# Optimization experiments

Hardware: AMD Instinct MI355X
Metric: run time of the kernel (lower is better)

## Reference

```python
import jax, jax.numpy as jnp
import numpy as np

B, LTEXT, LVIS, D, H = 16, 128, 4096, 1024, 16
HD = D // H


def setup_inputs() -> dict:
    key = jax.random.key(0)
    ks = jax.random.split(key, 8)
    s = 0.02
    return {
        'hidden_states': jax.random.normal(ks[0], (B, LVIS, D), jnp.float32),
        'text_states': jax.random.normal(ks[1], (LTEXT, B, D), jnp.float32),
        'Wq': jax.random.normal(ks[2], (D, D), jnp.float32) * s,
        'bq': jnp.zeros((D,), jnp.float32),
        'Wk': jax.random.normal(ks[3], (D, D), jnp.float32) * s,
        'bk': jnp.zeros((D,), jnp.float32),
        'Wv': jax.random.normal(ks[4], (D, D), jnp.float32) * s,
        'bv': jnp.zeros((D,), jnp.float32),
        'Wo': jax.random.normal(ks[5], (D, D), jnp.float32) * s,
        'bo': jnp.zeros((D,), jnp.float32),
    }


def reference(hidden_states, text_states, Wq, bq, Wk, bk, Wv, bv, Wo, bo):
    # text_states: (L_text, B, D) -- code unpacks text_len, bsz from dims 0,1
    # hidden_states: (B, L_vis, D) -- key/value source
    Ltext, bsz, d = text_states.shape
    Lvis = hidden_states.shape[1]
    scale = HD ** -0.5

    # projections (torch Linear x @ W.T + b, here W stored already transposed)
    q = (text_states @ Wq + bq) * scale
    # faithful to torch .view: flatten memory then reshape to (B, Ltext, H, hd)
    q = q.reshape(bsz, Ltext, H, HD).transpose(0, 2, 1, 3)        # (B,H,Lt,hd)
    k = (hidden_states @ Wk + bk).reshape(bsz, Lvis, H, HD).transpose(0, 2, 1, 3)
    v = (hidden_states @ Wv + bv).reshape(bsz, Lvis, H, HD).transpose(0, 2, 1, 3)

    attn = jax.nn.softmax(jnp.einsum('bhtd,bhsd->bhts', q, k), axis=-1)  # (B,H,Lt,Lv)
    text_guided_vision = jnp.einsum('bhts,bhsd->bhtd', attn, v)          # (B,H,Lt,hd)
    # second matmul with transposed attention weights: P^T @ (P V)
    out = jnp.einsum('bhts,bhtd->bhsd', attn, text_guided_vision)        # (B,H,Lv,hd)

    out = out.transpose(0, 2, 1, 3).reshape(bsz, Lvis, d)
    return out @ Wo + bo
```

## Files before the change

### kernel.cpp

```cpp
#include <hip/hip_runtime.h>
#include <stdint.h>

typedef short  s16x8 __attribute__((ext_vector_type(8)));
typedef float  f32x4 __attribute__((ext_vector_type(4)));
typedef unsigned short u16x4 __attribute__((ext_vector_type(4)));

__device__ __forceinline__ unsigned short f2bf(float f) {
  unsigned u = __builtin_bit_cast(unsigned, f);
  u = (u + 0x7fffu + ((u >> 16) & 1u)) >> 16;
  return (unsigned short)u;
}

__device__ __forceinline__ void glds16(const void* g, void* l) {
  __builtin_amdgcn_global_load_lds((const __attribute__((address_space(1))) void*)g,
                                   (__attribute__((address_space(3))) void*)l, 16, 0, 0);
}

__device__ __forceinline__ f32x4 mfma16(s16x8 a, s16x8 b, f32x4 c) {
  return __builtin_amdgcn_mfma_f32_16x16x32_bf16(a, b, c, 0, 0, 0);
}

#define VM4 asm volatile("s_waitcnt vmcnt(4)" ::: "memory")
#define VM0 asm volatile("s_waitcnt vmcnt(0)" ::: "memory")

__global__ __launch_bounds__(256) void kt_cvt(const float* __restrict__ X,
                                              unsigned short* __restrict__ Y) {
  const size_t N8 = (size_t)16 * 4096 * 1024 / 8;
  for (size_t i = (size_t)blockIdx.x * 256 + threadIdx.x; i < N8;
       i += (size_t)gridDim.x * 256) {
    const float* g = X + i * 8;
    f32x4 a = *(const f32x4*)g;
    f32x4 b = *(const f32x4*)(g + 4);
    s16x8 o;
    o[0]=f2bf(a[0]); o[1]=f2bf(a[1]); o[2]=f2bf(a[2]); o[3]=f2bf(a[3]);
    o[4]=f2bf(b[0]); o[5]=f2bf(b[1]); o[6]=f2bf(b[2]); o[7]=f2bf(b[3]);
    *(s16x8*)(Y + i * 8) = o;
  }
}

__global__ void kt_transpose(const float* __restrict__ W, unsigned short* __restrict__ WT) {
  __shared__ float tile[64][65];
  int n0 = blockIdx.x * 64, k0 = blockIdx.y * 64;
  int tx = threadIdx.x, ty = threadIdx.y;
  #pragma unroll
  for (int r = ty; r < 64; r += 4)
    tile[r][tx] = W[(size_t)(k0 + r) * 1024 + n0 + tx];
  __syncthreads();
  #pragma unroll
  for (int r = ty; r < 64; r += 4)
    WT[(size_t)(n0 + r) * 1024 + k0 + tx] = f2bf(tile[tx][r]);
}

__global__ __launch_bounds__(256, 2) void kt_gemm_q(
    const float* __restrict__ Ain, const unsigned short* __restrict__ BT,
    const float* __restrict__ bias, unsigned short* __restrict__ Cout) {
  __shared__ __align__(16) unsigned short As[128 * 32];
  __shared__ __align__(16) unsigned short Bs[128 * 32];
  const int tid = threadIdx.x, lane = tid & 63, wave = tid >> 6;
  const int l15 = lane & 15, quad = lane >> 4;
  const int wr = wave >> 1, wc = wave & 1;
  const int n0 = blockIdx.x * 128, m0 = blockIdx.y * 128;

  f32x4 acc[4][4] = {};
  for (int k0 = 0; k0 < 1024; k0 += 32) {
    __syncthreads();
    #pragma unroll
    for (int i = 0; i < 2; ++i) {
      int rowb = (wave * 2 + i) * 16 + (lane >> 2);
      glds16(BT + (size_t)(n0 + rowb) * 1024 + k0 + (lane & 3) * 8,
             &Bs[(wave * 2 + i) * 512]);
    }
    {
      const float* A = Ain;
      int row = tid >> 1, ks = (tid & 1) * 16;
      const float* g = &A[(size_t)(m0 + row) * 1024 + k0 + ks];
      f32x4 fa = *(const f32x4*)(g);
      f32x4 fb = *(const f32x4*)(g + 4);
      f32x4 fc = *(const f32x4*)(g + 8);
      f32x4 fd = *(const f32x4*)(g + 12);
      s16x8 lo, hi;
      lo[0]=f2bf(fa[0]); lo[1]=f2bf(fa[1]); lo[2]=f2bf(fa[2]); lo[3]=f2bf(fa[3]);
      lo[4]=f2bf(fb[0]); lo[5]=f2bf(fb[1]); lo[6]=f2bf(fb[2]); lo[7]=f2bf(fb[3]);
      hi[0]=f2bf(fc[0]); hi[1]=f2bf(fc[1]); hi[2]=f2bf(fc[2]); hi[3]=f2bf(fc[3]);
      hi[4]=f2bf(fd[0]); hi[5]=f2bf(fd[1]); hi[6]=f2bf(fd[2]); hi[7]=f2bf(fd[3]);
      *(s16x8*)&As[row * 32 + ks] = lo;
      *(s16x8*)&As[row * 32 + ks + 8] = hi;
    }
    __syncthreads();
    s16x8 a[4], b[4];
    #pragma unroll
    for (int i = 0; i < 4; ++i) a[i] = *(const s16x8*)&As[(wr * 64 + i * 16 + l15) * 32 + quad * 8];
    #pragma unroll
    for (int j = 0; j < 4; ++j) b[j] = *(const s16x8*)&Bs[(wc * 64 + j * 16 + l15) * 32 + quad * 8];
    #pragma unroll
    for (int i = 0; i < 4; ++i)
      #pragma unroll
      for (int j = 0; j < 4; ++j) acc[i][j] = mfma16(a[i], b[j], acc[i][j]);
  }
  #pragma unroll
  for (int j = 0; j < 4; ++j) {
    int col = n0 + wc * 64 + j * 16 + l15;
    float bv = bias[col];
    #pragma unroll
    for (int i = 0; i < 4; ++i)
      #pragma unroll
      for (int r = 0; r < 4; ++r) {
        int row = m0 + wr * 64 + i * 16 + quad * 4 + r;
        float v = (acc[i][j][r] + bv) * 0.125f;
        size_t idx = ((size_t)((row >> 7) * 16 + (col >> 6)) * 128 + (row & 127)) * 64 + (col & 63);
        Cout[idx] = f2bf(v);
      }
  }
}

template <int MODE>
__global__ __launch_bounds__(512, 2) void kt_gemm256(
    const unsigned short* __restrict__ A, const unsigned short* __restrict__ BT,
    const float* __restrict__ bias, void* __restrict__ Cout) {
  __shared__ __align__(16) unsigned short lds[65536];
  const int tid = threadIdx.x, lane = tid & 63, wave = tid >> 6;
  const int l15 = lane & 15, quad = lane >> 4;
  const int wr = wave >> 2, wc = wave & 3;
  const int r0 = lane >> 3, sck = (lane & 7) ^ r0;
  const int nblk = blockIdx.x & 3, mblk = blockIdx.x >> 2;
  const int n0 = nblk * 256, m0 = mblk * 256;
  const unsigned short* Asrc = A + (size_t)m0 * 1024;
  const unsigned short* Bsrc = BT + (size_t)n0 * 1024;

  f32x4 acc[8][4] = {};
  s16x8 bf_[4][2];

  auto stageA = [&](int t, int h, int buf) {
    #pragma unroll
    for (int is = 0; is < 2; ++is) {
      int c = wave * 2 + is;
      glds16(Asrc + (size_t)(h * 128 + c * 8 + r0) * 1024 + t * 64 + sck * 8,
             &lds[buf * 32768 + h * 8192 + c * 512]);
    }
  };
  auto stageB = [&](int t, int h, int buf) {
    #pragma unroll
    for (int is = 0; is < 2; ++is) {
      int c = wave * 2 + is;
      glds16(Bsrc + (size_t)(h * 128 + c * 8 + r0) * 1024 + t * 64 + sck * 8,
             &lds[buf * 32768 + 16384 + h * 8192 + c * 512]);
    }
  };

  stageA(0, 0, 0); stageA(0, 1, 0); stageB(0, 0, 0); stageB(0, 1, 0);
  stageB(1, 0, 1); stageB(1, 1, 1);
  VM4;
  __builtin_amdgcn_s_barrier();

  #pragma unroll 1
  for (int it = 0; it < 8; ++it) {
    const bool last = (it == 7);
    const int te = 2 * it;
    #pragma unroll
    for (int half = 0; half < 2; ++half) {
      const int buf = half;
      #pragma unroll
      for (int p = 0; p < 4; ++p) {
        if (p == 0) {
          #pragma unroll
          for (int j = 0; j < 4; ++j)
            #pragma unroll
            for (int kk = 0; kk < 2; ++kk) {
              int r = (wc & 1) * 64 + j * 16 + l15;
              bf_[j][kk] = *(const s16x8*)&lds[buf * 32768 + 16384 + (wc >> 1) * 8192
                                               + r * 64 + (((kk * 4 + quad) ^ (r & 7)) << 3)];
            }
        }
        s16x8 af[2][2];
        #pragma unroll
        for (int ii = 0; ii < 2; ++ii)
          #pragma unroll
          for (int kk = 0; kk < 2; ++kk) {
            int r = (p * 2 + ii) * 16 + l15;
            af[ii][kk] = *(const s16x8*)&lds[buf * 32768 + wr * 8192
                                             + r * 64 + (((kk * 4 + quad) ^ (r & 7)) << 3)];
          }
        if (half == 0) {
          if (p == 0) { stageA(te + 1, 0, 1); stageA(te + 1, 1, 1); }
          else if (p == 1) { if (!last) stageB(te + 2, 0, 0); }
          else if (p == 2) { if (!last) stageB(te + 2, 1, 0); }
        } else {
          if (p == 0) { if (!last) stageA(te + 2, 0, 0); }
          else if (p == 1) { if (!last) { stageA(te + 2, 1, 0); stageB(te + 3, 0, 1); } }
          else if (p == 2) { if (!last) stageB(te + 3, 1, 1); }
        }
        __builtin_amdgcn_s_barrier();
        __builtin_amdgcn_s_setprio(1);
        #pragma unroll
        for (int ii = 0; ii < 2; ++ii)
          #pragma unroll
          for (int j = 0; j < 4; ++j)
            #pragma unroll
            for (int kk = 0; kk < 2; ++kk)
              acc[p * 2 + ii][j] = mfma16(af[ii][kk], bf_[j][kk], acc[p * 2 + ii][j]);
        __builtin_amdgcn_s_setprio(0);
        if (p == 3) {
          if (half == 0) { if (last) { VM0; } else { VM4; } }
          else           { if (!last) { VM4; } }
        }
        __builtin_amdgcn_s_barrier();
      }
    }
  }

  const int bb = m0 >> 12;
  #pragma unroll
  for (int j = 0; j < 4; ++j) {
    const int col = n0 + wc * 64 + j * 16 + l15;
    const float bv = bias[col];
    const int hcol = col >> 6, dcol = col & 63;
    #pragma unroll
    for (int i = 0; i < 8; ++i) {
      const int row0 = m0 + wr * 128 + i * 16 + quad * 4;
      const int s = row0 & 4095;
      if constexpr (MODE == 0) {
        unsigned short* Ko = (unsigned short*)Cout;
        size_t base = (((size_t)bb * 16 + hcol) * 4096 + s) * 64 + dcol;
        #pragma unroll
        for (int r = 0; r < 4; ++r) Ko[base + (size_t)r * 64] = f2bf(acc[i][j][r] + bv);
      } else if constexpr (MODE == 1) {
        size_t base = (((size_t)bb * 16 + hcol) * 64 + dcol) * 4096 + s;
        u16x4 w;
        #pragma unroll
        for (int r = 0; r < 4; ++r) w[r] = f2bf(acc[i][j][r] + bv);
        *(u16x4*)&((unsigned short*)Cout)[base] = w;
      } else {
        float* O = (float*)Cout;
        size_t base = (size_t)row0 * 1024 + col;
        #pragma unroll
        for (int r = 0; r < 4; ++r) O[base + (size_t)r * 1024] = acc[i][j][r] + bv;
      }
    }
  }
}

__global__ __launch_bounds__(256, 2) void kt_attn1(
    const unsigned short* __restrict__ Qb, const unsigned short* __restrict__ Kb,
    const unsigned short* __restrict__ Vt, float* __restrict__ RpT,
    float* __restrict__ Zp) {
  __shared__ __align__(16) unsigned short Ks[128 * 64];
  __shared__ __align__(16) unsigned short Vts[64 * 128];
  __shared__ __align__(16) unsigned short Es[128 * 128];
  const int tid = threadIdx.x, lane = tid & 63, wave = tid >> 6;
  const int l15 = lane & 15, quad = lane >> 4;
  const int qidx = blockIdx.x, h = blockIdx.y, b = blockIdx.z;
  const int bh = b * 16 + h;
  const size_t kbase = (size_t)bh * 4096 * 64;
  const size_t vbase = (size_t)bh * 64 * 4096;
  s16x8 qa[2][2];
  #pragma unroll
  for (int i = 0; i < 2; ++i)
    #pragma unroll
    for (int kk = 0; kk < 2; ++kk)
      qa[i][kk] = *(const s16x8*)&Qb[((size_t)bh * 128 + wave * 32 + i * 16 + l15) * 64 + kk * 32 + quad * 8];
  s16x8 bones;
  { unsigned short o = (l15 == 0) ? (unsigned short)0x3F80 : (unsigned short)0;
    #pragma unroll
    for (int c2 = 0; c2 < 8; ++c2) bones[c2] = (short)o; }
  f32x4 Racc[2][4] = {};
  f32x4 Zacc[2] = {};
  for (int ch = 0; ch < 8; ++ch) {
    const int s0 = qidx * 1024 + ch * 128;
    __syncthreads();
    #pragma unroll
    for (int i = 0; i < 4; ++i) {
      int srow = (wave * 4 + i) * 8 + (lane >> 3);
      glds16(Kb + kbase + (size_t)(s0 + srow) * 64 + (lane & 7) * 8, &Ks[(wave * 4 + i) * 512]);
    }
    #pragma unroll
    for (int i = 0; i < 4; ++i) {
      int drow = (wave * 4 + i) * 4 + (lane >> 4);
      glds16(Vt + vbase + (size_t)drow * 4096 + s0 + (lane & 15) * 8, &Vts[(wave * 4 + i) * 512]);
    }
    __syncthreads();
    f32x4 Sacc[2][8] = {};
    #pragma unroll
    for (int kk = 0; kk < 2; ++kk) {
      s16x8 bk_[8];
      #pragma unroll
      for (int j = 0; j < 8; ++j)
        bk_[j] = *(const s16x8*)&Ks[(j * 16 + l15) * 64 + kk * 32 + quad * 8];
      #pragma unroll
      for (int i = 0; i < 2; ++i)
        #pragma unroll
        for (int j = 0; j < 8; ++j) Sacc[i][j] = mfma16(qa[i][kk], bk_[j], Sacc[i][j]);
    }
    #pragma unroll
    for (int i = 0; i < 2; ++i)
      #pragma unroll
      for (int j = 0; j < 8; ++j)
        #pragma unroll
        for (int r = 0; r < 4; ++r)
          Es[(wave * 32 + i * 16 + quad * 4 + r) * 128 + j * 16 + l15] = f2bf(__expf(Sacc[i][j][r]));
    #pragma unroll
    for (int kk = 0; kk < 4; ++kk) {
      s16x8 ea[2];
      #pragma unroll
      for (int i2 = 0; i2 < 2; ++i2)
        ea[i2] = *(const s16x8*)&Es[(wave * 32 + i2 * 16 + l15) * 128 + kk * 32 + quad * 8];
      s16x8 bv_[4];
      #pragma unroll
      for (int jd = 0; jd < 4; ++jd)
        bv_[jd] = *(const s16x8*)&Vts[(jd * 16 + l15) * 128 + kk * 32 + quad * 8];
      #pragma unroll
      for (int i2 = 0; i2 < 2; ++i2) {
        #pragma unroll
        for (int jd = 0; jd < 4; ++jd) Racc[i2][jd] = mfma16(ea[i2], bv_[jd], Racc[i2][jd]);
        Zacc[i2] = mfma16(ea[i2], bones, Zacc[i2]);
      }
    }
  }
  #pragma unroll
  for (int i2 = 0; i2 < 2; ++i2) {
    int t0 = wave * 32 + i2 * 16 + quad * 4;
    #pragma unroll
    for (int jd = 0; jd < 4; ++jd) {
      int d = jd * 16 + l15;
      *(f32x4*)&RpT[(((size_t)qidx * 256 + bh) * 64 + d) * 128 + t0] = Racc[i2][jd];
    }
    if (l15 == 0) {
      #pragma unroll
      for (int r = 0; r < 4; ++r)
        Zp[((size_t)qidx * 256 + bh) * 128 + t0 + r] = Zacc[i2][r];
    }
  }
}

__global__ void kt_reduce(const float* __restrict__ RpT, const float* __restrict__ Zp,
                          unsigned short* __restrict__ Gt) {
  size_t id = (size_t)blockIdx.x * 256 + threadIdx.x;
  int t = (int)(id & 127);
  size_t bh = id >> 13;
  float z = 0.f, r = 0.f;
  #pragma unroll
  for (int q = 0; q < 4; ++q) {
    z += Zp[(size_t)q * 32768 + bh * 128 + t];
    r += RpT[(size_t)q * 2097152 + id];
  }
  Gt[id] = f2bf(r / (z * z));
}

__global__ __launch_bounds__(256, 2) void kt_attn2(
    const unsigned short* __restrict__ Qb, const unsigned short* __restrict__ Kb,
    const unsigned short* __restrict__ Gt, unsigned short* __restrict__ Ao) {
  __shared__ __align__(16) unsigned short Ks[64 * 64];
  __shared__ __align__(16) unsigned short EsT[64 * 136];
  const int tid = threadIdx.x, lane = tid & 63, wave = tid >> 6;
  const int l15 = lane & 15, quad = lane >> 4;
  const int c = blockIdx.x, h = blockIdx.y, b = blockIdx.z;
  const int bh = b * 16 + h;
  s16x8 qf[8][2], gf[4][4];
  #pragma unroll
  for (int jt = 0; jt < 8; ++jt)
    #pragma unroll
    for (int kk = 0; kk < 2; ++kk)
      qf[jt][kk] = *(const s16x8*)&Qb[((size_t)bh * 128 + jt * 16 + l15) * 64 + kk * 32 + quad * 8];
  #pragma unroll
  for (int jd = 0; jd < 4; ++jd)
    #pragma unroll
    for (int kk = 0; kk < 4; ++kk)
      gf[jd][kk] = *(const s16x8*)&Gt[((size_t)bh * 64 + jd * 16 + l15) * 128 + kk * 32 + quad * 8];
  const size_t kbase = (size_t)bh * 4096 * 64;
  for (int it = 0; it < 16; ++it) {
    const int s0 = c * 1024 + it * 64;
    __syncthreads();
    #pragma unroll
    for (int i = 0; i < 2; ++i) {
      int srow = (wave * 2 + i) * 8 + (lane >> 3);
      glds16(Kb + kbase + (size_t)(s0 + srow) * 64 + (lane & 7) * 8, &Ks[(wave * 2 + i) * 512]);
    }
    __syncthreads();
    f32x4 Sacc[8] = {};
    #pragma unroll
    for (int kk = 0; kk < 2; ++kk) {
      s16x8 a = *(const s16x8*)&Ks[(wave * 16 + l15) * 64 + kk * 32 + quad * 8];
      #pragma unroll
      for (int jt = 0; jt < 8; ++jt) Sacc[jt] = mfma16(a, qf[jt][kk], Sacc[jt]);
    }
    #pragma unroll
    for (int jt = 0; jt < 8; ++jt)
      #pragma unroll
      for (int r = 0; r < 4; ++r)
        EsT[(wave * 16 + quad * 4 + r) * 136 + jt * 16 + l15] = f2bf(__expf(Sacc[jt][r]));
    f32x4 Oacc[4] = {};
    #pragma unroll
    for (int kk = 0; kk < 4; ++kk) {
      s16x8 ea = *(const s16x8*)&EsT[(wave * 16 + l15) * 136 + kk * 32 + quad * 8];
      #pragma unroll
      for (int jd = 0; jd < 4; ++jd) Oacc[jd] = mfma16(ea, gf[jd][kk], Oacc[jd]);
    }
    #pragma unroll
    for (int jd = 0; jd < 4; ++jd)
      #pragma unroll
      for (int r = 0; r < 4; ++r) {
        int s = s0 + wave * 16 + quad * 4 + r;
        int d = jd * 16 + l15;
        Ao[((size_t)b * 4096 + s) * 1024 + h * 64 + d] = f2bf(Oacc[jd][r]);
      }
  }
}

extern "C" void kernel_launch(void* const* d_in, const int* in_sizes, int n_in,
                              void* d_out, int out_size, void* d_ws, size_t ws_size,
                              hipStream_t stream) {
  const float* hidden = (const float*)d_in[0];
  const float* text   = (const float*)d_in[1];
  const float* Wq = (const float*)d_in[2]; const float* bq = (const float*)d_in[3];
  const float* Wk = (const float*)d_in[4]; const float* bk = (const float*)d_in[5];
  const float* Wv = (const float*)d_in[6]; const float* bv = (const float*)d_in[7];
  const float* Wo = (const float*)d_in[8]; const float* bo = (const float*)d_in[9];
  char* ws = (char*)d_ws;
  unsigned short* WqT = (unsigned short*)(ws + (size_t)0);
  unsigned short* WkT = (unsigned short*)(ws + ((size_t)2 << 20));
  unsigned short* WvT = (unsigned short*)(ws + ((size_t)4 << 20));
  unsigned short* WoT = (unsigned short*)(ws + ((size_t)6 << 20));
  unsigned short* Qb  = (unsigned short*)(ws + ((size_t)8 << 20));
  unsigned short* Kb  = (unsigned short*)(ws + ((size_t)12 << 20));
  unsigned short* Vt  = (unsigned short*)(ws + ((size_t)140 << 20));
  unsigned short* Hb  = (unsigned short*)(ws + ((size_t)268 << 20));
  unsigned short* Ao  = (unsigned short*)(ws + ((size_t)268 << 20));
  float*          RpT = (float*)(ws + ((size_t)396 << 20));
  float*          Zp  = (float*)(ws + ((size_t)428 << 20));
  unsigned short* Gt  = (unsigned short*)(ws + ((size_t)429 << 20));

  dim3 blk(256);
  kt_transpose<<<dim3(16, 16), dim3(64, 4), 0, stream>>>(Wq, WqT);
  kt_transpose<<<dim3(16, 16), dim3(64, 4), 0, stream>>>(Wk, WkT);
  kt_transpose<<<dim3(16, 16), dim3(64, 4), 0, stream>>>(Wv, WvT);
  kt_transpose<<<dim3(16, 16), dim3(64, 4), 0, stream>>>(Wo, WoT);
  kt_cvt<<<dim3(2048), blk, 0, stream>>>(hidden, Hb);
  kt_gemm_q<<<dim3(8, 16), blk, 0, stream>>>(text, WqT, bq, Qb);
  kt_gemm256<0><<<dim3(1024), dim3(512), 0, stream>>>(Hb, WkT, bk, Kb);
  kt_gemm256<1><<<dim3(1024), dim3(512), 0, stream>>>(Hb, WvT, bv, Vt);
  kt_attn1<<<dim3(4, 16, 16), blk, 0, stream>>>(Qb, Kb, Vt, RpT, Zp);
  kt_reduce<<<dim3(8192), blk, 0, stream>>>(RpT, Zp, Gt);
  kt_attn2<<<dim3(4, 16, 16), blk, 0, stream>>>(Qb, Kb, Gt, Ao);
  kt_gemm256<2><<<dim3(1024), dim3(512), 0, stream>>>(Ao, WoT, bo, d_out);
}
```

Before: 1.193 ms.

## Fuse K/V projection GEMMs and remap blocks to XCDs for cache locality

```diff
diff --git a/kernel.cpp b/kernel.cpp
--- a/kernel.cpp
+++ b/kernel.cpp
@@ -116,13 +116,18 @@
 template <int MODE>
 __global__ __launch_bounds__(512, 2) void kt_gemm256(
     const unsigned short* __restrict__ A, const unsigned short* __restrict__ BT,
-    const float* __restrict__ bias, void* __restrict__ Cout) {
+    const float* __restrict__ bias0, const float* __restrict__ bias1,
+    void* __restrict__ out0, void* __restrict__ out1) {
+  constexpr int NN = (MODE == 0) ? 8 : 4;
+  constexpr int CHUNK = (MODE == 0) ? 256 : 128;
   __shared__ __align__(16) unsigned short lds[65536];
   const int tid = threadIdx.x, lane = tid & 63, wave = tid >> 6;
   const int l15 = lane & 15, quad = lane >> 4;
   const int wr = wave >> 2, wc = wave & 3;
   const int r0 = lane >> 3, sck = (lane & 7) ^ r0;
-  const int nblk = blockIdx.x & 3, mblk = blockIdx.x >> 2;
+  const int bid = blockIdx.x;
+  const int logical = (bid & 7) * CHUNK + (bid >> 3);
+  const int nblk = logical & (NN - 1), mblk = logical / NN;
   const int n0 = nblk * 256, m0 = mblk * 256;
   const unsigned short* Asrc = A + (size_t)m0 * 1024;
   const unsigned short* Bsrc = BT + (size_t)n0 * 1024;
@@ -209,29 +214,34 @@
   }
 
   const int bb = m0 >> 12;
+  const bool isV = (MODE == 0) && (n0 >= 1024);
+  const float* bias = isV ? bias1 : bias0;
   #pragma unroll
   for (int j = 0; j < 4; ++j) {
-    const int col = n0 + wc * 64 + j * 16 + l15;
-    const float bv = bias[col];
-    const int hcol = col >> 6, dcol = col & 63;
+    const int colg = n0 + wc * 64 + j * 16 + l15;
+    const int c1 = colg & 1023;
+    const float bv = bias[c1];
+    const int hcol = c1 >> 6, dcol = c1 & 63;
     #pragma unroll
     for (int i = 0; i < 8; ++i) {
       const int row0 = m0 + wr * 128 + i * 16 + quad * 4;
       const int s = row0 & 4095;
       if constexpr (MODE == 0) {
-        unsigned short* Ko = (unsigned short*)Cout;
-        size_t base = (((size_t)bb * 16 + hcol) * 4096 + s) * 64 + dcol;
-        #pragma unroll
-        for (int r = 0; r < 4; ++r) Ko[base + (size_t)r * 64] = f2bf(acc[i][j][r] + bv);
-      } else if constexpr (MODE == 1) {
-        size_t base = (((size_t)bb * 16 + hcol) * 64 + dcol) * 4096 + s;
-        u16x4 w;
-        #pragma unroll
-        for (int r = 0; r < 4; ++r) w[r] = f2bf(acc[i][j][r] + bv);
-        *(u16x4*)&((unsigned short*)Cout)[base] = w;
+        if (isV) {
+          size_t base = (((size_t)bb * 16 + hcol) * 64 + dcol) * 4096 + s;
+          u16x4 w;
+          #pragma unroll
+          for (int r = 0; r < 4; ++r) w[r] = f2bf(acc[i][j][r] + bv);
+          *(u16x4*)&((unsigned short*)out1)[base] = w;
+        } else {
+          unsigned short* Ko = (unsigned short*)out0;
+          size_t base = (((size_t)bb * 16 + hcol) * 4096 + s) * 64 + dcol;
+          #pragma unroll
+          for (int r = 0; r < 4; ++r) Ko[base + (size_t)r * 64] = f2bf(acc[i][j][r] + bv);
+        }
       } else {
-        float* O = (float*)Cout;
-        size_t base = (size_t)row0 * 1024 + col;
+        float* O = (float*)out0;
+        size_t base = (size_t)row0 * 1024 + colg;
         #pragma unroll
         for (int r = 0; r < 4; ++r) O[base + (size_t)r * 1024] = acc[i][j][r] + bv;
       }
@@ -248,8 +258,9 @@
   __shared__ __align__(16) unsigned short Es[128 * 128];
   const int tid = threadIdx.x, lane = tid & 63, wave = tid >> 6;
   const int l15 = lane & 15, quad = lane >> 4;
-  const int qidx = blockIdx.x, h = blockIdx.y, b = blockIdx.z;
-  const int bh = b * 16 + h;
+  const int bid = blockIdx.x;
+  const int lid = (bid & 7) * 128 + (bid >> 3);
+  const int qidx = lid & 3, bh = lid >> 2;
   const size_t kbase = (size_t)bh * 4096 * 64;
   const size_t vbase = (size_t)bh * 64 * 4096;
   s16x8 qa[2][2];
@@ -352,8 +363,10 @@
   __shared__ __align__(16) unsigned short EsT[64 * 136];
   const int tid = threadIdx.x, lane = tid & 63, wave = tid >> 6;
   const int l15 = lane & 15, quad = lane >> 4;
-  const int c = blockIdx.x, h = blockIdx.y, b = blockIdx.z;
-  const int bh = b * 16 + h;
+  const int bid = blockIdx.x;
+  const int lid = (bid & 7) * 128 + (bid >> 3);
+  const int c = lid & 3, bh = lid >> 2;
+  const int h = bh & 15, b = bh >> 4;
   s16x8 qf[8][2], gf[4][4];
   #pragma unroll
   for (int jt = 0; jt < 8; ++jt)
@@ -435,10 +448,9 @@
   kt_transpose<<<dim3(16, 16), dim3(64, 4), 0, stream>>>(Wo, WoT);
   kt_cvt<<<dim3(2048), blk, 0, stream>>>(hidden, Hb);
   kt_gemm_q<<<dim3(8, 16), blk, 0, stream>>>(text, WqT, bq, Qb);
-  kt_gemm256<0><<<dim3(1024), dim3(512), 0, stream>>>(Hb, WkT, bk, Kb);
-  kt_gemm256<1><<<dim3(1024), dim3(512), 0, stream>>>(Hb, WvT, bv, Vt);
-  kt_attn1<<<dim3(4, 16, 16), blk, 0, stream>>>(Qb, Kb, Vt, RpT, Zp);
+  kt_gemm256<0><<<dim3(2048), dim3(512), 0, stream>>>(Hb, WkT, bk, bv, Kb, Vt);
+  kt_attn1<<<dim3(1024), blk, 0, stream>>>(Qb, Kb, Vt, RpT, Zp);
   kt_reduce<<<dim3(8192), blk, 0, stream>>>(RpT, Zp, Gt);
-  kt_attn2<<<dim3(4, 16, 16), blk, 0, stream>>>(Qb, Kb, Gt, Ao);
-  kt_gemm256<2><<<dim3(1024), dim3(512), 0, stream>>>(Ao, WoT, bo, d_out);
-}
+  kt_attn2<<<dim3(1024), blk, 0, stream>>>(Qb, Kb, Gt, Ao);
+  kt_gemm256<2><<<dim3(1024), dim3(512), 0, stream>>>(Ao, WoT, bo, nullptr, d_out, nullptr);
+}
```

Measured after the change: 1.196 ms. Within noise of the previous version (+0.2%).
